# Performance work log

Hardware: AMD Instinct MI355X
Metric: run time of the kernel (lower is better)

The kernel has to match this reference:

```python
import jax, jax.numpy as jnp
import numpy as np

B, D, E, K = 8192, 4096, 64, 2

def setup_inputs() -> dict:
    key = jax.random.key(0)
    k1, k2 = jax.random.split(key)
    x = jax.random.normal(k1, (B, D), dtype=jnp.float32)
    gate_w = jax.random.normal(k2, (E, D), dtype=jnp.float32) * (1.0 / np.sqrt(D))
    temperature = jnp.ones((), dtype=jnp.float32)
    return {"x": x, "gate_w": gate_w, "temperature": temperature}

def reference(x, gate_w, temperature):
    # logits = (x @ W^T) / temperature  -> [B, E]
    logits = jnp.einsum('bd,ed->be', x, gate_w) / temperature
    top_logits, top_idx = jax.lax.top_k(logits, K)          # [B, K]
    routing_weights = jax.nn.softmax(top_logits, axis=-1)    # [B, K]
    rows = jnp.arange(x.shape[0])[:, None]                   # [B, 1]
    routing_matrix = jnp.zeros((x.shape[0], E), dtype=x.dtype).at[rows, top_idx].set(routing_weights)
    return routing_matrix, top_idx
```

## Files before the change

### kernel.cpp

```cpp
#include <hip/hip_runtime.h>
#include <stdint.h>
#include <stddef.h>


typedef __attribute__((ext_vector_type(8))) short short8;
typedef __attribute__((ext_vector_type(4))) float f32x4;

static constexpr int kB = 8192;
static constexpr int kD = 4096;
static constexpr int kE = 64;
static constexpr int kSteps = kD / 32;
static constexpr int kWv = 8;
static constexpr int kSPC = kSteps / kWv;
static constexpr int kRows = 16;

__device__ __forceinline__ uint32_t bf16_rne(float v) {
    uint32_t u = __builtin_bit_cast(uint32_t, v);
    return (u + 0x7FFFu + ((u >> 16) & 1u)) >> 16;
}

__device__ __forceinline__ void cvt8(const f32x4& a0, const f32x4& a1,
                                     short8& ah, short8& al) {
#pragma unroll
    for (int j = 0; j < 4; ++j) {
        float xv = a0[j];
        uint32_t u  = __builtin_bit_cast(uint32_t, xv);
        uint32_t rh = (u + 0x7FFFu + ((u >> 16) & 1u)) & 0xFFFF0000u;
        ah[j] = (short)(rh >> 16);
        al[j] = (short)bf16_rne(xv - __builtin_bit_cast(float, rh));
        float yv = a1[j];
        uint32_t u2  = __builtin_bit_cast(uint32_t, yv);
        uint32_t rh2 = (u2 + 0x7FFFu + ((u2 >> 16) & 1u)) & 0xFFFF0000u;
        ah[j + 4] = (short)(rh2 >> 16);
        al[j + 4] = (short)bf16_rne(yv - __builtin_bit_cast(float, rh2));
    }
}

__global__ __launch_bounds__(256) void prep_w_kernel(
    const float* __restrict__ w, short* __restrict__ w_hi, short* __restrict__ w_lo)
{
    int tid  = blockIdx.x * 256 + threadIdx.x;
    int lane = tid & 63;
    int s    = (tid >> 6) & (kSteps - 1);
    int nt   = tid >> 13;
    int e = nt * 16 + (lane & 15);
    int k = s * 32 + (lane >> 4) * 8;
    const float* src = w + (size_t)e * kD + k;
    short8 hi, lo;
#pragma unroll
    for (int j = 0; j < 8; ++j) {
        float xv = src[j];
        uint32_t u  = __builtin_bit_cast(uint32_t, xv);
        uint32_t rh = (u + 0x7FFFu + ((u >> 16) & 1u)) & 0xFFFF0000u;
        hi[j] = (short)(rh >> 16);
        float lf = xv - __builtin_bit_cast(float, rh);
        lo[j] = (short)bf16_rne(lf);
    }
    ((short8*)w_hi)[tid] = hi;
    ((short8*)w_lo)[tid] = lo;
}

__global__ __launch_bounds__(512, 4) void router_kernel(
    const float* __restrict__ x, const short8* __restrict__ w_hi,
    const short8* __restrict__ w_lo, const float* __restrict__ temp,
    float* __restrict__ out_mat, float* __restrict__ out_idx)
{
    const int lane = threadIdx.x & 63;
    const int wv   = threadIdx.x >> 6;
    const int quad = lane >> 4;
    const int mr   = lane & 15;
    const int row0 = blockIdx.x * kRows;

    const float* xp = x + (size_t)(row0 + mr) * kD + wv * (kSPC * 32) + quad * 8;

    f32x4 acc[4];
#pragma unroll
    for (int nt = 0; nt < 4; ++nt) acc[nt] = (f32x4){0.f, 0.f, 0.f, 0.f};

    f32x4 xb[2][2][2];
#pragma unroll
    for (int st = 0; st < 2; ++st) {
        const f32x4* ap = (const f32x4*)(xp + st * 32);
        xb[0][st][0] = ap[0];
        xb[0][st][1] = ap[1];
    }

    for (int g = 0; g < kSPC / 2; ++g) {
        const int cur = g & 1, nxt = cur ^ 1;
        if (g + 1 < kSPC / 2) {
#pragma unroll
            for (int st = 0; st < 2; ++st) {
                const f32x4* ap = (const f32x4*)(xp + ((g + 1) * 2 + st) * 32);
                xb[nxt][st][0] = ap[0];
                xb[nxt][st][1] = ap[1];
            }
        }
#pragma unroll
        for (int st = 0; st < 2; ++st) {
            short8 ah, al;
            cvt8(xb[cur][st][0], xb[cur][st][1], ah, al);
            const size_t sb = (size_t)(wv * kSPC + g * 2 + st) * 64 + lane;
#pragma unroll
            for (int nt = 0; nt < 4; ++nt) {
                short8 wh_ = w_hi[(size_t)(nt * kSteps) * 64 + sb];
                short8 wl_ = w_lo[(size_t)(nt * kSteps) * 64 + sb];
                acc[nt] = __builtin_amdgcn_mfma_f32_16x16x32_bf16(al, wl_, acc[nt], 0, 0, 0);
                acc[nt] = __builtin_amdgcn_mfma_f32_16x16x32_bf16(al, wh_, acc[nt], 0, 0, 0);
                acc[nt] = __builtin_amdgcn_mfma_f32_16x16x32_bf16(ah, wl_, acc[nt], 0, 0, 0);
                acc[nt] = __builtin_amdgcn_mfma_f32_16x16x32_bf16(ah, wh_, acc[nt], 0, 0, 0);
            }
        }
    }

    __shared__ float part[kWv][kRows][kE];
#pragma unroll
    for (int nt = 0; nt < 4; ++nt)
#pragma unroll
        for (int r = 0; r < 4; ++r)
            part[wv][quad * 4 + r][nt * 16 + mr] = acc[nt][r];
    __syncthreads();

    const float invT = 1.0f / temp[0];
#pragma unroll
    for (int p = 0; p < 2; ++p) {
        const int row = wv + p * kWv;
        float v = 0.f;
#pragma unroll
        for (int s = 0; s < kWv; ++s)
            v += part[s][row][lane];

        float v1 = v; int i1 = lane;
#pragma unroll
        for (int m = 1; m < 64; m <<= 1) {
            float ov = __shfl_xor(v1, m, 64);
            int   oi = __shfl_xor(i1, m, 64);
            if (ov > v1 || (ov == v1 && oi < i1)) { v1 = ov; i1 = oi; }
        }
        float vm = (lane == i1) ? -3.0e38f : v;
        float v2 = vm; int i2 = lane;
#pragma unroll
        for (int m = 1; m < 64; m <<= 1) {
            float ov = __shfl_xor(v2, m, 64);
            int   oi = __shfl_xor(i2, m, 64);
            if (ov > v2 || (ov == v2 && oi < i2)) { v2 = ov; i2 = oi; }
        }

        float e  = expf((v2 - v1) * invT);
        float sm = 1.0f + e;
        out_mat[(size_t)(row0 + row) * kE + lane] =
            (lane == i1) ? (1.0f / sm) : ((lane == i2) ? (e / sm) : 0.0f);
        if (lane == 0)
            ((float2*)out_idx)[row0 + row] = make_float2((float)i1, (float)i2);
    }
}

extern "C" void kernel_launch(void* const* d_in, const int* in_sizes, int n_in,
                              void* d_out, int out_size, void* d_ws, size_t ws_size,
                              hipStream_t stream) {
    const float* x    = (const float*)d_in[0];
    const float* gw   = (const float*)d_in[1];
    const float* temp = (const float*)d_in[2];

    float* out_mat = (float*)d_out;
    float* out_idx = (float*)d_out + (size_t)kB * kE;

    short* w_hi = (short*)d_ws;
    short* w_lo = w_hi + (size_t)kE * kD;

    prep_w_kernel<<<128, 256, 0, stream>>>(gw, w_hi, w_lo);

    router_kernel<<<kB / kRows, 512, 0, stream>>>(
        x, (const short8*)w_hi, (const short8*)w_lo, temp, out_mat, out_idx);
}
```

Baseline: 213.5 us.

## Stage x tiles into LDS via direct global-to-LDS loads with double buffering

Each block now loads its 16-row x slab in 256-column chunks with global_load_lds straight into a double-buffered, padded LDS tile. Each wave then reads its 32-column fragment from LDS rather than streaming its own contiguous K range from global memory. Weight fragments are register double-buffered in step with the chunks, and the reduction scratch reuses the same LDS. The aim is coalesced row-contiguous global reads of x and overlap of loads with MFMA. In exchange it adds a block-wide barrier every chunk and more LDS per block, which may reduce occupancy.

```diff
diff --git a/kernel.cpp b/kernel.cpp
--- a/kernel.cpp
+++ b/kernel.cpp
@@ -11,8 +11,10 @@
 static constexpr int kE = 64;
 static constexpr int kSteps = kD / 32;
 static constexpr int kWv = 8;
-static constexpr int kSPC = kSteps / kWv;
 static constexpr int kRows = 16;
+static constexpr int kBK = 256;
+static constexpr int kBufs = kD / kBK;
+static constexpr int kRowPad = 260;
 
 __device__ __forceinline__ uint32_t bf16_rne(float v) {
     uint32_t u = __builtin_bit_cast(uint32_t, v);
@@ -34,6 +36,12 @@
         ah[j + 4] = (short)(rh2 >> 16);
         al[j + 4] = (short)bf16_rne(yv - __builtin_bit_cast(float, rh2));
     }
+}
+
+__device__ __forceinline__ void glds16(const float* g, float* l) {
+    __builtin_amdgcn_global_load_lds(
+        (const __attribute__((address_space(1))) unsigned int*)g,
+        (__attribute__((address_space(3))) unsigned int*)l, 16, 0, 0);
 }
 
 __global__ __launch_bounds__(256) void prep_w_kernel(
@@ -71,48 +79,63 @@
     const int mr   = lane & 15;
     const int row0 = blockIdx.x * kRows;
 
-    const float* xp = x + (size_t)(row0 + mr) * kD + wv * (kSPC * 32) + quad * 8;
+    __shared__ __align__(16) float smem[2 * kRows * kRowPad];
+    float (*lds_x)[kRows][kRowPad] = (float (*)[kRows][kRowPad])smem;
+    float (*part)[kRows][kE]       = (float (*)[kRows][kE])smem;
 
     f32x4 acc[4];
 #pragma unroll
     for (int nt = 0; nt < 4; ++nt) acc[nt] = (f32x4){0.f, 0.f, 0.f, 0.f};
 
-    f32x4 xb[2][2][2];
+    short8 wbh[2][4], wbl[2][4];
+
 #pragma unroll
-    for (int st = 0; st < 2; ++st) {
-        const f32x4* ap = (const f32x4*)(xp + st * 32);
-        xb[0][st][0] = ap[0];
-        xb[0][st][1] = ap[1];
+    for (int seg = 0; seg < 2; ++seg) {
+        const int r = 2 * wv + seg;
+        glds16(x + (size_t)(row0 + r) * kD + lane * 4, &lds_x[0][r][0]);
+    }
+#pragma unroll
+    for (int nt = 0; nt < 4; ++nt) {
+        wbh[0][nt] = w_hi[(size_t)(nt * kSteps + wv) * 64 + lane];
+        wbl[0][nt] = w_lo[(size_t)(nt * kSteps + wv) * 64 + lane];
     }
 
-    for (int g = 0; g < kSPC / 2; ++g) {
-        const int cur = g & 1, nxt = cur ^ 1;
-        if (g + 1 < kSPC / 2) {
+#pragma unroll 2
+    for (int b = 0; b < kBufs; ++b) {
+        const int pb = b & 1;
+        __syncthreads();
+
+        if (b + 1 < kBufs) {
 #pragma unroll
-            for (int st = 0; st < 2; ++st) {
-                const f32x4* ap = (const f32x4*)(xp + ((g + 1) * 2 + st) * 32);
-                xb[nxt][st][0] = ap[0];
-                xb[nxt][st][1] = ap[1];
+            for (int seg = 0; seg < 2; ++seg) {
+                const int r = 2 * wv + seg;
+                glds16(x + (size_t)(row0 + r) * kD + (b + 1) * kBK + lane * 4,
+                       &lds_x[pb ^ 1][r][0]);
+            }
+            const int s = (b + 1) * kWv + wv;
+#pragma unroll
+            for (int nt = 0; nt < 4; ++nt) {
+                wbh[pb ^ 1][nt] = w_hi[(size_t)(nt * kSteps + s) * 64 + lane];
+                wbl[pb ^ 1][nt] = w_lo[(size_t)(nt * kSteps + s) * 64 + lane];
             }
         }
+
+        const float* ap = &lds_x[pb][mr][wv * 32 + quad * 8];
+        f32x4 a0 = *(const f32x4*)ap;
+        f32x4 a1 = *(const f32x4*)(ap + 4);
+        short8 ah, al;
+        cvt8(a0, a1, ah, al);
 #pragma unroll
-        for (int st = 0; st < 2; ++st) {
-            short8 ah, al;
-            cvt8(xb[cur][st][0], xb[cur][st][1], ah, al);
-            const size_t sb = (size_t)(wv * kSPC + g * 2 + st) * 64 + lane;
-#pragma unroll
-            for (int nt = 0; nt < 4; ++nt) {
-                short8 wh_ = w_hi[(size_t)(nt * kSteps) * 64 + sb];
-                short8 wl_ = w_lo[(size_t)(nt * kSteps) * 64 + sb];
-                acc[nt] = __builtin_amdgcn_mfma_f32_16x16x32_bf16(al, wl_, acc[nt], 0, 0, 0);
-                acc[nt] = __builtin_amdgcn_mfma_f32_16x16x32_bf16(al, wh_, acc[nt], 0, 0, 0);
-                acc[nt] = __builtin_amdgcn_mfma_f32_16x16x32_bf16(ah, wl_, acc[nt], 0, 0, 0);
-                acc[nt] = __builtin_amdgcn_mfma_f32_16x16x32_bf16(ah, wh_, acc[nt], 0, 0, 0);
-            }
+        for (int nt = 0; nt < 4; ++nt) {
+            acc[nt] = __builtin_amdgcn_mfma_f32_16x16x32_bf16(al, wbl[pb][nt], acc[nt], 0, 0, 0);
+            acc[nt] = __builtin_amdgcn_mfma_f32_16x16x32_bf16(al, wbh[pb][nt], acc[nt], 0, 0, 0);
+            acc[nt] = __builtin_amdgcn_mfma_f32_16x16x32_bf16(ah, wbl[pb][nt], acc[nt], 0, 0, 0);
+            acc[nt] = __builtin_amdgcn_mfma_f32_16x16x32_bf16(ah, wbh[pb][nt], acc[nt], 0, 0, 0);
         }
     }
 
-    __shared__ float part[kWv][kRows][kE];
+    __syncthreads();
+
 #pragma unroll
     for (int nt = 0; nt < 4; ++nt)
 #pragma unroll
```

Result: faster. 204.3 us (-4.3%).

## Split GEMM into row-group/K-split partial kernel plus separate reduce-top2 kernel

Applied to the files above, without the earlier changes.

Restructures the router. Previously each block handled 16 rows and split K across 8 waves, reducing through LDS. Now each block takes 128 rows (8 waves × 16 rows) over one K-slice, so the weight tiles loaded per block are reused across more rows, and weight loads are double-buffered in registers alongside x. Partial sums go to a global workspace of 8×B×E floats, and a second kernel reduces them and does the top-2 softmax. This adds extra global traffic (about 16MB written and read back) and an extra kernel launch. Only 512 GEMM blocks are launched, which may under-fill the GPU.

```diff
diff --git a/kernel.cpp b/kernel.cpp
--- a/kernel.cpp
+++ b/kernel.cpp
@@ -10,9 +10,10 @@
 static constexpr int kD = 4096;
 static constexpr int kE = 64;
 static constexpr int kSteps = kD / 32;
-static constexpr int kWv = 8;
-static constexpr int kSPC = kSteps / kWv;
-static constexpr int kRows = 16;
+static constexpr int kKS = 8;
+static constexpr int kSPS = kSteps / kKS;
+static constexpr int kRG = 64;
+static constexpr int kRPB = kB / kRG;
 
 __device__ __forceinline__ uint32_t bf16_rne(float v) {
     uint32_t u = __builtin_bit_cast(uint32_t, v);
@@ -60,74 +61,88 @@
     ((short8*)w_lo)[tid] = lo;
 }
 
-__global__ __launch_bounds__(512, 4) void router_kernel(
+__global__ __launch_bounds__(512, 4) void gemm_partial(
     const float* __restrict__ x, const short8* __restrict__ w_hi,
-    const short8* __restrict__ w_lo, const float* __restrict__ temp,
-    float* __restrict__ out_mat, float* __restrict__ out_idx)
+    const short8* __restrict__ w_lo, float* __restrict__ part)
 {
     const int lane = threadIdx.x & 63;
-    const int wv   = threadIdx.x >> 6;
+    const int mt   = threadIdx.x >> 6;
     const int quad = lane >> 4;
     const int mr   = lane & 15;
-    const int row0 = blockIdx.x * kRows;
+    const int ks   = blockIdx.x >> 6;
+    const int rg   = blockIdx.x & 63;
 
-    const float* xp = x + (size_t)(row0 + mr) * kD + wv * (kSPC * 32) + quad * 8;
+    const int row0 = rg * kRPB + mt * 16;
+    const float* xp = x + (size_t)(row0 + mr) * kD + ks * (kSPS * 32) + quad * 8;
 
     f32x4 acc[4];
 #pragma unroll
     for (int nt = 0; nt < 4; ++nt) acc[nt] = (f32x4){0.f, 0.f, 0.f, 0.f};
 
-    f32x4 xb[2][2][2];
+    f32x4  xb[2][2];
+    short8 wbh[2][4], wbl[2][4];
+
 #pragma unroll
-    for (int st = 0; st < 2; ++st) {
-        const f32x4* ap = (const f32x4*)(xp + st * 32);
-        xb[0][st][0] = ap[0];
-        xb[0][st][1] = ap[1];
+    for (int s = 0; s < 2; ++s) {
+        const f32x4* ap = (const f32x4*)(xp + s * 32);
+        xb[s][0] = ap[0];
+        xb[s][1] = ap[1];
+        const size_t S = (size_t)(ks * kSPS + s);
+#pragma unroll
+        for (int nt = 0; nt < 4; ++nt) {
+            wbh[s][nt] = w_hi[(size_t)(nt * kSteps) * 64 + S * 64 + lane];
+            wbl[s][nt] = w_lo[(size_t)(nt * kSteps) * 64 + S * 64 + lane];
+        }
     }
 
-    for (int g = 0; g < kSPC / 2; ++g) {
-        const int cur = g & 1, nxt = cur ^ 1;
-        if (g + 1 < kSPC / 2) {
 #pragma unroll
-            for (int st = 0; st < 2; ++st) {
-                const f32x4* ap = (const f32x4*)(xp + ((g + 1) * 2 + st) * 32);
-                xb[nxt][st][0] = ap[0];
-                xb[nxt][st][1] = ap[1];
-            }
+    for (int s = 0; s < kSPS; ++s) {
+        const int slot = s & 1;
+        short8 ah, al;
+        cvt8(xb[slot][0], xb[slot][1], ah, al);
+#pragma unroll
+        for (int nt = 0; nt < 4; ++nt) {
+            acc[nt] = __builtin_amdgcn_mfma_f32_16x16x32_bf16(al, wbl[slot][nt], acc[nt], 0, 0, 0);
+            acc[nt] = __builtin_amdgcn_mfma_f32_16x16x32_bf16(al, wbh[slot][nt], acc[nt], 0, 0, 0);
+            acc[nt] = __builtin_amdgcn_mfma_f32_16x16x32_bf16(ah, wbl[slot][nt], acc[nt], 0, 0, 0);
+            acc[nt] = __builtin_amdgcn_mfma_f32_16x16x32_bf16(ah, wbh[slot][nt], acc[nt], 0, 0, 0);
         }
-#pragma unroll
-        for (int st = 0; st < 2; ++st) {
-            short8 ah, al;
-            cvt8(xb[cur][st][0], xb[cur][st][1], ah, al);
-            const size_t sb = (size_t)(wv * kSPC + g * 2 + st) * 64 + lane;
+        if (s + 2 < kSPS) {
+            const f32x4* ap = (const f32x4*)(xp + (s + 2) * 32);
+            xb[slot][0] = ap[0];
+            xb[slot][1] = ap[1];
+            const size_t S = (size_t)(ks * kSPS + s + 2);
 #pragma unroll
             for (int nt = 0; nt < 4; ++nt) {
-                short8 wh_ = w_hi[(size_t)(nt * kSteps) * 64 + sb];
-                short8 wl_ = w_lo[(size_t)(nt * kSteps) * 64 + sb];
-                acc[nt] = __builtin_amdgcn_mfma_f32_16x16x32_bf16(al, wl_, acc[nt], 0, 0, 0);
-                acc[nt] = __builtin_amdgcn_mfma_f32_16x16x32_bf16(al, wh_, acc[nt], 0, 0, 0);
-                acc[nt] = __builtin_amdgcn_mfma_f32_16x16x32_bf16(ah, wl_, acc[nt], 0, 0, 0);
-                acc[nt] = __builtin_amdgcn_mfma_f32_16x16x32_bf16(ah, wh_, acc[nt], 0, 0, 0);
+                wbh[slot][nt] = w_hi[(size_t)(nt * kSteps) * 64 + S * 64 + lane];
+                wbl[slot][nt] = w_lo[(size_t)(nt * kSteps) * 64 + S * 64 + lane];
             }
         }
     }
 
-    __shared__ float part[kWv][kRows][kE];
+    float* pp = part + ((size_t)ks * kB + row0) * kE;
 #pragma unroll
     for (int nt = 0; nt < 4; ++nt)
 #pragma unroll
         for (int r = 0; r < 4; ++r)
-            part[wv][quad * 4 + r][nt * 16 + mr] = acc[nt][r];
-    __syncthreads();
+            pp[(size_t)(quad * 4 + r) * kE + nt * 16 + mr] = acc[nt][r];
+}
 
+__global__ __launch_bounds__(256) void reduce_top2(
+    const float* __restrict__ part, const float* __restrict__ temp,
+    float* __restrict__ out_mat, float* __restrict__ out_idx)
+{
+    const int lane = threadIdx.x & 63;
+    const int wv   = threadIdx.x >> 6;
     const float invT = 1.0f / temp[0];
+
 #pragma unroll
-    for (int p = 0; p < 2; ++p) {
-        const int row = wv + p * kWv;
+    for (int i = 0; i < 4; ++i) {
+        const int row = blockIdx.x * 16 + wv * 4 + i;
         float v = 0.f;
 #pragma unroll
-        for (int s = 0; s < kWv; ++s)
-            v += part[s][row][lane];
+        for (int ks = 0; ks < kKS; ++ks)
+            v += part[((size_t)ks * kB + row) * kE + lane];
 
         float v1 = v; int i1 = lane;
 #pragma unroll
@@ -147,10 +162,10 @@
 
         float e  = expf((v2 - v1) * invT);
         float sm = 1.0f + e;
-        out_mat[(size_t)(row0 + row) * kE + lane] =
+        out_mat[(size_t)row * kE + lane] =
             (lane == i1) ? (1.0f / sm) : ((lane == i2) ? (e / sm) : 0.0f);
         if (lane == 0)
-            ((float2*)out_idx)[row0 + row] = make_float2((float)i1, (float)i2);
+            ((float2*)out_idx)[row] = make_float2((float)i1, (float)i2);
     }
 }
 
@@ -166,9 +181,12 @@
 
     short* w_hi = (short*)d_ws;
     short* w_lo = w_hi + (size_t)kE * kD;
+    float* part = (float*)(w_lo + (size_t)kE * kD);
 
     prep_w_kernel<<<128, 256, 0, stream>>>(gw, w_hi, w_lo);
 
-    router_kernel<<<kB / kRows, 512, 0, stream>>>(
-        x, (const short8*)w_hi, (const short8*)w_lo, temp, out_mat, out_idx);
+    gemm_partial<<<kRG * kKS, 512, 0, stream>>>(
+        x, (const short8*)w_hi, (const short8*)w_lo, part);
+
+    reduce_top2<<<512, 256, 0, stream>>>(part, temp, out_mat, out_idx);
 }
```

After: 218.9 us. +2.5%, slower.
